# Optimization experiments

Hardware: AMD Instinct MI355X
Metric: run time of the kernel (lower is better)

The kernel has to match this reference:

```python
import jax, jax.numpy as jnp
import numpy as np

K_MASK = -2.3819763e+38
B, T, D = 1, 2048, 3584
N, KH, H = 28, 4, 128  # query heads, kv heads, head_dim
ROPE_THETA = 1000000.0


def _rope_tables(t, h, theta):
    pos = jnp.arange(t, dtype=jnp.float32)[:, None]
    freq = theta ** (-jnp.arange(0, h, 2, dtype=jnp.float32) / h)[None, :]
    ang = pos * freq  # (T, H/2)
    return jnp.sin(ang)[None], jnp.cos(ang)[None]  # (1, T, H/2)


def apply_rotary_embedding(x, sin, cos):
    # x: (B,T,heads,H); sin/cos: (B,T,H/2)
    x1, x2 = x[..., : x.shape[-1] // 2], x[..., x.shape[-1] // 2 :]
    s, c = sin[:, :, None, :], cos[:, :, None, :]
    return jnp.concatenate([x1 * c - x2 * s, x2 * c + x1 * s], axis=-1)


def setup_inputs() -> dict:
    key = jax.random.key(0)
    ks = jax.random.split(key, 8)
    x = jax.random.normal(ks[0], (B, T, D), jnp.float32)
    attn_mask = jnp.tril(jnp.ones((T, T), jnp.bool_))[None]  # causal (B,T,S)
    sin, cos = _rope_tables(T, H, ROPE_THETA)
    std = 0.02
    wq = jax.random.normal(ks[1], (D, N, H), jnp.float32) * std
    wk = jax.random.normal(ks[2], (D, KH, H), jnp.float32) * std
    wv = jax.random.normal(ks[3], (D, KH, H), jnp.float32) * std
    wo = jax.random.normal(ks[4], (N, H, D), jnp.float32) * std
    q_bias = jax.random.normal(ks[5], (N * H,), jnp.float32) * std
    k_bias = jax.random.normal(ks[6], (KH * H,), jnp.float32) * std
    v_bias = jax.random.normal(ks[7], (KH * H,), jnp.float32) * std
    return {"x": x, "attn_mask": attn_mask, "sin": sin, "cos": cos,
            "wq": wq, "wk": wk, "wv": wv, "wo": wo,
            "q_bias": q_bias, "k_bias": k_bias, "v_bias": v_bias}


def reference(x, attn_mask, sin, cos, wq, wk, wv, wo, q_bias, k_bias, v_bias):
    b, t, _ = x.shape
    q = jnp.einsum('BTD,DNH->BTNH', x, wq) + q_bias.reshape(1, 1, N, H)
    k = jnp.einsum('BSD,DKH->BSKH', x, wk) + k_bias.reshape(1, 1, KH, H)
    v = jnp.einsum('BSD,DKH->BSKH', x, wv) + v_bias.reshape(1, 1, KH, H)
    q = apply_rotary_embedding(q, sin, cos)
    k = apply_rotary_embedding(k, sin, cos)
    g = N // KH  # GQA group size
    scale = H ** -0.5
    qg = q.reshape(b, t, KH, g, H)
    attn = jnp.einsum('BTHGD,BSHD->BHGTS', qg, k) * scale  # no KV repetition
    attn = attn.reshape(b, N, t, t)
    attn = jnp.where(attn_mask[:, None, :, :], attn, K_MASK)
    attn = jax.nn.softmax(attn.astype(jnp.float32), axis=-1).astype(k.dtype)
    attn = attn.reshape(b, KH, g, t, t)
    qkv = jnp.einsum('BHGTS,BSHD->BTHGD', attn, v).reshape(b, t, N, H)
    return jnp.einsum('BTNH,NHD->BTD', qkv, wo)
```

## Files before the change

kernel.cpp:

```cpp
#include <hip/hip_runtime.h>
#include <hip/hip_bf16.h>
#include <math.h>

#define Tn 2048
#define Dn 3584
#define NH 28
#define KHn 4
#define Hn 128
#define Gn 7
#define SCALE 0.08838834764831845f
#define LDC 4608
#define KOFF 3584
#define VOFF 4096
#define FBQ 128
#define FBS 64
#define MAXT 8
#define EXP_SHIFT 12.0f

typedef unsigned short u16;
typedef __attribute__((ext_vector_type(8))) short short8;
typedef __attribute__((ext_vector_type(4))) float floatx4;

__device__ __constant__ unsigned char QT_TAB[40] = {
    15,15,15,15, 14,14,14, 13,13,13, 12,12,12, 11,11,11,
    10,10, 9,9, 8,8, 7,7, 6, 5, 4, 3,
    14,10,6,2, 13,9,5,1, 12,8,4,0};
__device__ __constant__ unsigned char S_TAB[40] = {
     0, 1, 2, 3,  0, 1, 2,  0, 1, 2,  0, 1, 2,  0, 1, 2,
     0, 1, 0,1, 0,1, 0,1, 0, 0, 0, 0,
     3, 2,1,0,  3,2,1,0,  3,2,1,0};

__device__ __forceinline__ float bf_lo(unsigned int u) {
    union { unsigned int i; float f; } x; x.i = u << 16; return x.f;
}
__device__ __forceinline__ u16 f2bf(float f) {
    __hip_bfloat16 h = __float2bfloat16(f);
    return *reinterpret_cast<u16*>(&h);
}

__global__ void cast_f32_bf16(const float* __restrict__ in, u16* __restrict__ out, int n4)
{
    const int idx = blockIdx.x * blockDim.x + threadIdx.x;
    if (idx >= n4) return;
    const float4 f = ((const float4*)in)[idx];
    ((ushort4*)out)[idx] = make_ushort4(f2bf(f.x), f2bf(f.y), f2bf(f.z), f2bf(f.w));
}

__global__ void zero_f32(float* __restrict__ p, int n)
{
    const int i = blockIdx.x * blockDim.x + threadIdx.x;
    if (i < n) p[i] = 0.f;
}

__global__ __launch_bounds__(256) void transpose_cast(
    const float* __restrict__ in, u16* __restrict__ out, int R, int C, int ldo)
{
    __shared__ float ts[32][33];
    const int tid = threadIdx.x;
    const int c0 = blockIdx.x * 32, r0 = blockIdx.y * 32;
    const int tx = tid & 31, ty = tid >> 5;
    #pragma unroll
    for (int i = 0; i < 4; ++i)
        ts[ty + i * 8][tx] = in[(size_t)(r0 + ty + i * 8) * C + c0 + tx];
    __syncthreads();
    #pragma unroll
    for (int i = 0; i < 4; ++i)
        out[(size_t)(c0 + ty + i * 8) * ldo + r0 + tx] = f2bf(ts[tx][ty + i * 8]);
}

__global__ __launch_bounds__(256) void transpose_v(
    const u16* __restrict__ qkv, u16* __restrict__ vt)
{
    __shared__ u16 ts[32][33];
    const int tid = threadIdx.x;
    const int s0 = blockIdx.x * 32, d0 = blockIdx.y * 32;
    const int tx = tid & 31, ty = tid >> 5;
    #pragma unroll
    for (int i = 0; i < 4; ++i)
        ts[ty + i * 8][tx] = qkv[(size_t)(s0 + ty + i * 8) * LDC + VOFF + d0 + tx];
    __syncthreads();
    #pragma unroll
    for (int i = 0; i < 4; ++i)
        vt[(size_t)(d0 + ty + i * 8) * Tn + s0 + tx] = ts[tx][ty + i * 8];
}

__global__ void concat_bias(const float* __restrict__ qb, const float* __restrict__ kb,
                            const float* __restrict__ vb, float* __restrict__ out)
{
    const int j = blockIdx.x * blockDim.x + threadIdx.x;
    if (j >= 4608) return;
    out[j] = j < 3584 ? qb[j] : (j < 4096 ? kb[j - 3584] : vb[j - 4096]);
}

#define GM 128
#define GN 128
#define GK 32

__device__ __forceinline__ void async16(const void* g, void* l) {
    __builtin_amdgcn_global_load_lds(
        (const __attribute__((address_space(1))) unsigned int*)g,
        (__attribute__((address_space(3))) unsigned int*)l, 16, 0, 0);
}

template <typename OUT_T>
__global__ __launch_bounds__(256) void gemm_bf16_mfma(
    const u16* __restrict__ A, const u16* __restrict__ Bt,
    const float* __restrict__ bias, OUT_T* __restrict__ C,
    int M, int N, int K, int ldc)
{
    __shared__ __align__(16) u16 As[GM * GK];
    __shared__ __align__(16) u16 Bs[GN * GK];

    const int tid  = threadIdx.x;
    const int lane = tid & 63;
    const int wave = tid >> 6;
    const int wr = wave >> 1, wc = wave & 1;
    const int m16 = lane & 15, quad = lane >> 4;

    const int nwg = gridDim.x * gridDim.y;
    const int bid = blockIdx.y * gridDim.x + blockIdx.x;
    const int cpx = nwg >> 3;
    const int swz = (bid & 7) * cpx + (bid >> 3);
    const int bm = (swz / gridDim.x) * GM;
    const int bn = (swz % gridDim.x) * GN;

    floatx4 acc[4][4];
    #pragma unroll
    for (int i = 0; i < 4; ++i)
        #pragma unroll
        for (int j = 0; j < 4; ++j) acc[i][j] = (floatx4)0.f;

    const int rl   = lane >> 2;
    const int kcol = (lane & 3) * 8;

    for (int k0 = 0; k0 < K; k0 += GK) {
        __syncthreads();
        #pragma unroll
        for (int i = 0; i < 2; ++i) {
            const int c = wave + i * 4;
            const int row = c * 16 + rl;
            async16(A  + (size_t)(bm + row) * K + k0 + kcol, &As[c * 512]);
            async16(Bt + (size_t)(bn + row) * K + k0 + kcol, &Bs[c * 512]);
        }
        __builtin_amdgcn_s_waitcnt(0);
        __syncthreads();

        short8 af[4], bfr[4];
        #pragma unroll
        for (int i = 0; i < 4; ++i)
            af[i] = *(const short8*)&As[(wr * 64 + i * 16 + m16) * GK + quad * 8];
        #pragma unroll
        for (int j = 0; j < 4; ++j)
            bfr[j] = *(const short8*)&Bs[(wc * 64 + j * 16 + m16) * GK + quad * 8];
        #pragma unroll
        for (int i = 0; i < 4; ++i)
            #pragma unroll
            for (int j = 0; j < 4; ++j)
                acc[i][j] = __builtin_amdgcn_mfma_f32_16x16x32_bf16(
                    af[i], bfr[j], acc[i][j], 0, 0, 0);
    }

    #pragma unroll
    for (int j = 0; j < 4; ++j) {
        const int col = bn + wc * 64 + j * 16 + m16;
        const float bv = bias ? bias[col] : 0.f;
        #pragma unroll
        for (int i = 0; i < 4; ++i) {
            const int rbase = bm + wr * 64 + i * 16 + quad * 4;
            #pragma unroll
            for (int r = 0; r < 4; ++r) {
                const float v = acc[i][j][r] + bv;
                if constexpr (sizeof(OUT_T) == 2)
                    C[(size_t)(rbase + r) * ldc + col] = (OUT_T)f2bf(v);
                else
                    C[(size_t)(rbase + r) * ldc + col] = v;
            }
        }
    }
}

__global__ void rope_bf16(u16* __restrict__ base,
                          const float* __restrict__ sin_t,
                          const float* __restrict__ cos_t,
                          int heads)
{
    const int idx = blockIdx.x * blockDim.x + threadIdx.x;
    const int n_elem = Tn * heads * 64;
    if (idx >= n_elem) return;
    const int i = idx & 63;
    const int h = (idx >> 6) % heads;
    const int t = idx / (64 * heads);
    const float s = sin_t[t * 64 + i];
    const float c = cos_t[t * 64 + i];
    u16* p = base + (size_t)t * LDC + h * Hn;
    const float x1 = bf_lo((unsigned int)p[i]);
    const float x2 = bf_lo((unsigned int)p[i + 64]);
    p[i]      = f2bf(x1 * c - x2 * s);
    p[i + 64] = f2bf(x2 * c + x1 * s);
}

__global__ __launch_bounds__(256, 2) void flash_attn_mfma(
    const u16* __restrict__ qkv, const u16* __restrict__ vt,
    u16* __restrict__ pb01, u16* __restrict__ pb23,
    float* __restrict__ lb)
{
    const int qt = (int)QT_TAB[blockIdx.x];
    const int s  = (int)S_TAB[blockIdx.x];
    const int n  = blockIdx.y;
    const int kh = n / Gn;
    const int tid  = threadIdx.x;
    const int lane = tid & 63;
    const int w    = tid >> 6;
    const int m16  = lane & 15;
    const int quad = lane >> 4;

    __shared__ __align__(16) u16 smem[64 * 136 + 128 * 72 + 128 * 72];
    u16* Ks = smem;
    u16* Vs = smem + 64 * 136;
    u16* Ps = Vs + 128 * 72;

    short8 qf[2][4];
    #pragma unroll
    for (int p = 0; p < 2; ++p) {
        const int qrow = qt * FBQ + w * 32 + p * 16 + m16;
        const u16* qp = qkv + (size_t)qrow * LDC + n * Hn;
        #pragma unroll
        for (int kc = 0; kc < 4; ++kc)
            qf[p][kc] = *(const short8*)(qp + kc * 32 + quad * 8);
    }

    floatx4 oacc[2][8];
    #pragma unroll
    for (int p = 0; p < 2; ++p)
        #pragma unroll
        for (int jn = 0; jn < 8; ++jn) oacc[p][jn] = (floatx4)0.f;
    float lrow[2][4];
    #pragma unroll
    for (int p = 0; p < 2; ++p)
        #pragma unroll
        for (int r = 0; r < 4; ++r) lrow[p][r] = 0.f;

    const int krow = tid >> 2, kseg = tid & 3;
    const int vrow = tid >> 1, vseg = tid & 1;
    const int nst = 2 * qt + 2;
    const int st0 = s * MAXT;
    const int st1 = (st0 + MAXT < nst) ? st0 + MAXT : nst;

    uint4 kv[4], vv[4];
    {
        const u16* kp = qkv + (size_t)(st0 * FBS + krow) * LDC + KOFF + kh * Hn + kseg * 32;
        #pragma unroll
        for (int i = 0; i < 4; ++i) kv[i] = *(const uint4*)(kp + i * 8);
        const u16* vp = vt + (size_t)(kh * Hn + vrow) * Tn + st0 * FBS + vseg * 32;
        #pragma unroll
        for (int i = 0; i < 4; ++i) vv[i] = *(const uint4*)(vp + i * 8);
    }

    for (int st = st0; st < st1; ++st) {
        __syncthreads();
        #pragma unroll
        for (int i = 0; i < 4; ++i)
            *(uint4*)&Ks[krow * 136 + kseg * 32 + i * 8] = kv[i];
        #pragma unroll
        for (int i = 0; i < 4; ++i)
            *(uint4*)&Vs[vrow * 72 + vseg * 32 + i * 8] = vv[i];
        __syncthreads();

        {
            const int pst = (st + 1 < st1) ? st + 1 : st1 - 1;
            const u16* kp = qkv + (size_t)(pst * FBS + krow) * LDC + KOFF + kh * Hn + kseg * 32;
            #pragma unroll
            for (int i = 0; i < 4; ++i) kv[i] = *(const uint4*)(kp + i * 8);
            const u16* vp = vt + (size_t)(kh * Hn + vrow) * Tn + pst * FBS + vseg * 32;
            #pragma unroll
            for (int i = 0; i < 4; ++i) vv[i] = *(const uint4*)(vp + i * 8);
        }

        const bool active = (st * FBS) <= (qt * FBQ + w * 32 + 31);
        if (active) {
            floatx4 sacc[2][4];
            #pragma unroll
            for (int p = 0; p < 2; ++p)
                #pragma unroll
                for (int j = 0; j < 4; ++j) sacc[p][j] = (floatx4)0.f;
            #pragma unroll
            for (int j = 0; j < 4; ++j) {
                #pragma unroll
                for (int kc = 0; kc < 4; ++kc) {
                    const short8 bfv = *(const short8*)&Ks[(j * 16 + m16) * 136 + kc * 32 + quad * 8];
                    sacc[0][j] = __builtin_amdgcn_mfma_f32_16x16x32_bf16(qf[0][kc], bfv, sacc[0][j], 0, 0, 0);
                    sacc[1][j] = __builtin_amdgcn_mfma_f32_16x16x32_bf16(qf[1][kc], bfv, sacc[1][j], 0, 0, 0);
                }
            }

            const bool diag = (st >= 2 * qt);
            #pragma unroll
            for (int p = 0; p < 2; ++p) {
                #pragma unroll
                for (int r = 0; r < 4; ++r) {
                    const int prow = w * 32 + p * 16 + quad * 4 + r;
                    const int row  = qt * FBQ + prow;
                    float ls = 0.f;
                    #pragma unroll
                    for (int j = 0; j < 4; ++j) {
                        float sv = sacc[p][j][r] * SCALE - EXP_SHIFT;
                        if (diag && (st * FBS + j * 16 + m16 > row)) sv = -1.0e30f;
                        const float e = __expf(sv);
                        ls += e;
                        Ps[prow * 72 + j * 16 + m16] = f2bf(e);
                    }
                    lrow[p][r] += ls;
                }
            }

            #pragma unroll
            for (int kc2 = 0; kc2 < 2; ++kc2) {
                const short8 af0 = *(const short8*)&Ps[(w * 32 + m16) * 72 + kc2 * 32 + quad * 8];
                const short8 af1 = *(const short8*)&Ps[(w * 32 + 16 + m16) * 72 + kc2 * 32 + quad * 8];
                #pragma unroll
                for (int jn = 0; jn < 8; ++jn) {
                    const short8 bfv = *(const short8*)&Vs[(jn * 16 + m16) * 72 + kc2 * 32 + quad * 8];
                    oacc[0][jn] = __builtin_amdgcn_mfma_f32_16x16x32_bf16(af0, bfv, oacc[0][jn], 0, 0, 0);
                    oacc[1][jn] = __builtin_amdgcn_mfma_f32_16x16x32_bf16(af1, bfv, oacc[1][jn], 0, 0, 0);
                }
            }
        }
    }

    float lsum[2][4], invl[2][4];
    #pragma unroll
    for (int p = 0; p < 2; ++p)
        #pragma unroll
        for (int r = 0; r < 4; ++r) {
            float l = lrow[p][r];
            l += __shfl_xor(l, 1); l += __shfl_xor(l, 2);
            l += __shfl_xor(l, 4); l += __shfl_xor(l, 8);
            lsum[p][r] = l;
            invl[p][r] = (l > 0.f) ? 1.0f / l : 0.f;
        }

    if (m16 == 0) {
        #pragma unroll
        for (int p = 0; p < 2; ++p)
            #pragma unroll
            for (int r = 0; r < 4; ++r) {
                const int row = qt * FBQ + w * 32 + p * 16 + quad * 4 + r;
                lb[((size_t)s * NH + n) * Tn + row] = lsum[p][r];
            }
    }

    u16* po = (s < 2) ? pb01 + (size_t)s * Tn * Dn
                      : pb23 + (size_t)(s - 2) * Tn * Dn;
    #pragma unroll
    for (int p = 0; p < 2; ++p)
        #pragma unroll
        for (int r = 0; r < 4; ++r) {
            const int grow = qt * FBQ + w * 32 + p * 16 + quad * 4 + r;
            u16* pr = po + (size_t)grow * Dn + n * Hn + m16;
            #pragma unroll
            for (int jn = 0; jn < 8; ++jn)
                pr[jn * 16] = f2bf(oacc[p][jn][r] * invl[p][r]);
        }
}

__global__ __launch_bounds__(256) void combine_splits(
    const u16* __restrict__ pb01, const u16* __restrict__ pb23,
    const float* __restrict__ lb, u16* __restrict__ ob)
{
    const int idx = blockIdx.x * blockDim.x + threadIdx.x;
    const int n4  = Tn * Dn / 4;
    if (idx >= n4) return;
    const int c4  = idx % (Dn / 4);
    const int row = idx / (Dn / 4);
    const int n   = (c4 * 4) >> 7;

    float den = 0.f, ax = 0.f, ay = 0.f, az = 0.f, aw = 0.f;
    #pragma unroll
    for (int s = 0; s < 4; ++s) {
        const float l = lb[((size_t)s * NH + n) * Tn + row];
        if (l > 0.f) {
            const u16* p = (s < 2) ? pb01 + (size_t)s * Tn * Dn
                                   : pb23 + (size_t)(s - 2) * Tn * Dn;
            const ushort4 v = ((const ushort4*)p)[idx];
            den += l;
            ax += l * bf_lo((unsigned int)v.x);
            ay += l * bf_lo((unsigned int)v.y);
            az += l * bf_lo((unsigned int)v.z);
            aw += l * bf_lo((unsigned int)v.w);
        }
    }
    const float inv = 1.0f / den;
    ushort4 o;
    o.x = f2bf(ax * inv);
    o.y = f2bf(ay * inv);
    o.z = f2bf(az * inv);
    o.w = f2bf(aw * inv);
    ((ushort4*)ob)[idx] = o;
}

extern "C" void kernel_launch(void* const* d_in, const int* in_sizes, int n_in,
                              void* d_out, int out_size, void* d_ws, size_t ws_size,
                              hipStream_t stream)
{
    const float* x      = (const float*)d_in[0];
    const float* sin_t  = (const float*)d_in[2];
    const float* cos_t  = (const float*)d_in[3];
    const float* wq     = (const float*)d_in[4];
    const float* wk     = (const float*)d_in[5];
    const float* wv     = (const float*)d_in[6];
    const float* wo     = (const float*)d_in[7];
    const float* q_bias = (const float*)d_in[8];
    const float* k_bias = (const float*)d_in[9];
    const float* v_bias = (const float*)d_in[10];
    float* out = (float*)d_out;

    char* ws = (char*)d_ws;
    u16*  cqkv = (u16*)ws;
    u16*  abuf = (u16*)(ws + 18874368);
    u16*  wt   = (u16*)(ws + 18874368 + 14680064);
    float* bqkv = (float*)(ws + 66584576);
    u16*  vtg  = wt;
    u16*  pb01 = (u16*)d_out;
    u16*  pb23 = (u16*)(ws + 35651584);
    float* lbf = (float*)(ws + 65011712);
    u16*  xb   = (u16*)d_out;

    cast_f32_bf16<<<(Tn * Dn / 4 + 255) / 256, 256, 0, stream>>>(x, xb, Tn * Dn / 4);
    transpose_cast<<<dim3(Dn / 32, Dn / 32), 256, 0, stream>>>(wq, wt, Dn, Dn, Dn);
    transpose_cast<<<dim3(512 / 32, Dn / 32), 256, 0, stream>>>(wk, wt + (size_t)KOFF * Dn, Dn, 512, Dn);
    transpose_cast<<<dim3(512 / 32, Dn / 32), 256, 0, stream>>>(wv, wt + (size_t)VOFF * Dn, Dn, 512, Dn);
    concat_bias<<<18, 256, 0, stream>>>(q_bias, k_bias, v_bias, bqkv);

    gemm_bf16_mfma<u16><<<dim3(LDC / GN, Tn / GM), 256, 0, stream>>>(
        xb, wt, bqkv, cqkv, Tn, LDC, Dn, LDC);

    zero_f32<<<(4 * NH * Tn + 255) / 256, 256, 0, stream>>>(lbf, 4 * NH * Tn);

    rope_bf16<<<(Tn * 32 * 64 + 255) / 256, 256, 0, stream>>>(cqkv, sin_t, cos_t, 32);

    transpose_v<<<dim3(Tn / 32, 512 / 32), 256, 0, stream>>>(cqkv, vtg);

    flash_attn_mfma<<<dim3(40, NH), 256, 0, stream>>>(
        cqkv, vtg, pb01, pb23, lbf);

    combine_splits<<<(Tn * Dn / 4 + 255) / 256, 256, 0, stream>>>(pb01, pb23, lbf, abuf);

    transpose_cast<<<dim3(Dn / 32, Dn / 32), 256, 0, stream>>>(wo, wt, Dn, Dn, Dn);
    gemm_bf16_mfma<float><<<dim3(Dn / GN, Tn / GM), 256, 0, stream>>>(
        abuf, wt, nullptr, out, Tn, Dn, Dn, Dn);
}
```

Measured before the change: 562.2 us.

## Load K/V MFMA fragments directly from global and stage output stores through LDS

The flash-attention kernel no longer copies K and V tiles into shared memory. Each wave now loads its MFMA B-operand fragments straight from global memory, which removes the two per-tile __syncthreads and the register prefetch, and shrinks shared memory to the P buffer. The epilogue now writes normalized outputs into that P buffer per wave, then emits coalesced 16-byte row stores instead of scattered 2-byte stores. The cost is that all four waves re-fetch the same K/V data through the cache with strided, less coalesced accesses, and there is no explicit prefetch to hide that latency.

Result: slower. 579.0 us (+3.0%).

```diff
diff --git a/kernel.cpp b/kernel.cpp
--- a/kernel.cpp
+++ b/kernel.cpp
@@ -214,10 +214,7 @@
     const int m16  = lane & 15;
     const int quad = lane >> 4;
 
-    __shared__ __align__(16) u16 smem[64 * 136 + 128 * 72 + 128 * 72];
-    u16* Ks = smem;
-    u16* Vs = smem + 64 * 136;
-    u16* Ps = Vs + 128 * 72;
+    __shared__ __align__(16) u16 Ps[128 * 72];
 
     short8 qf[2][4];
     #pragma unroll
@@ -240,89 +237,63 @@
         #pragma unroll
         for (int r = 0; r < 4; ++r) lrow[p][r] = 0.f;
 
-    const int krow = tid >> 2, kseg = tid & 3;
-    const int vrow = tid >> 1, vseg = tid & 1;
     const int nst = 2 * qt + 2;
     const int st0 = s * MAXT;
     const int st1 = (st0 + MAXT < nst) ? st0 + MAXT : nst;
 
-    uint4 kv[4], vv[4];
-    {
-        const u16* kp = qkv + (size_t)(st0 * FBS + krow) * LDC + KOFF + kh * Hn + kseg * 32;
-        #pragma unroll
-        for (int i = 0; i < 4; ++i) kv[i] = *(const uint4*)(kp + i * 8);
-        const u16* vp = vt + (size_t)(kh * Hn + vrow) * Tn + st0 * FBS + vseg * 32;
-        #pragma unroll
-        for (int i = 0; i < 4; ++i) vv[i] = *(const uint4*)(vp + i * 8);
-    }
+    const u16* kfrag = qkv + (size_t)m16 * LDC + KOFF + kh * Hn + quad * 8;
+    const u16* vfrag = vt + (size_t)(kh * Hn + m16) * Tn + quad * 8;
 
     for (int st = st0; st < st1; ++st) {
-        __syncthreads();
-        #pragma unroll
-        for (int i = 0; i < 4; ++i)
-            *(uint4*)&Ks[krow * 136 + kseg * 32 + i * 8] = kv[i];
-        #pragma unroll
-        for (int i = 0; i < 4; ++i)
-            *(uint4*)&Vs[vrow * 72 + vseg * 32 + i * 8] = vv[i];
-        __syncthreads();
-
-        {
-            const int pst = (st + 1 < st1) ? st + 1 : st1 - 1;
-            const u16* kp = qkv + (size_t)(pst * FBS + krow) * LDC + KOFF + kh * Hn + kseg * 32;
-            #pragma unroll
-            for (int i = 0; i < 4; ++i) kv[i] = *(const uint4*)(kp + i * 8);
-            const u16* vp = vt + (size_t)(kh * Hn + vrow) * Tn + pst * FBS + vseg * 32;
-            #pragma unroll
-            for (int i = 0; i < 4; ++i) vv[i] = *(const uint4*)(vp + i * 8);
-        }
-
-        const bool active = (st * FBS) <= (qt * FBQ + w * 32 + 31);
-        if (active) {
-            floatx4 sacc[2][4];
-            #pragma unroll
-            for (int p = 0; p < 2; ++p)
+        if ((st * FBS) > (qt * FBQ + w * 32 + 31)) continue;
+
+        const u16* kb = kfrag + (size_t)(st * FBS) * LDC;
+        const u16* vb = vfrag + st * FBS;
+
+        floatx4 sacc[2][4];
+        #pragma unroll
+        for (int j = 0; j < 4; ++j) sacc[0][j] = (floatx4)0.f;
+        #pragma unroll
+        for (int j = 0; j < 4; ++j) sacc[1][j] = (floatx4)0.f;
+        #pragma unroll
+        for (int j = 0; j < 4; ++j) {
+            #pragma unroll
+            for (int kc = 0; kc < 4; ++kc) {
+                const short8 bfv = *(const short8*)(kb + (size_t)(j * 16) * LDC + kc * 32);
+                sacc[0][j] = __builtin_amdgcn_mfma_f32_16x16x32_bf16(qf[0][kc], bfv, sacc[0][j], 0, 0, 0);
+                sacc[1][j] = __builtin_amdgcn_mfma_f32_16x16x32_bf16(qf[1][kc], bfv, sacc[1][j], 0, 0, 0);
+            }
+        }
+
+        const bool diag = (st >= 2 * qt);
+        #pragma unroll
+        for (int p = 0; p < 2; ++p) {
+            #pragma unroll
+            for (int r = 0; r < 4; ++r) {
+                const int prow = w * 32 + p * 16 + quad * 4 + r;
+                const int row  = qt * FBQ + prow;
+                float ls = 0.f;
                 #pragma unroll
-                for (int j = 0; j < 4; ++j) sacc[p][j] = (floatx4)0.f;
-            #pragma unroll
-            for (int j = 0; j < 4; ++j) {
-                #pragma unroll
-                for (int kc = 0; kc < 4; ++kc) {
-                    const short8 bfv = *(const short8*)&Ks[(j * 16 + m16) * 136 + kc * 32 + quad * 8];
-                    sacc[0][j] = __builtin_amdgcn_mfma_f32_16x16x32_bf16(qf[0][kc], bfv, sacc[0][j], 0, 0, 0);
-                    sacc[1][j] = __builtin_amdgcn_mfma_f32_16x16x32_bf16(qf[1][kc], bfv, sacc[1][j], 0, 0, 0);
+                for (int j = 0; j < 4; ++j) {
+                    float sv = sacc[p][j][r] * SCALE - EXP_SHIFT;
+                    if (diag && (st * FBS + j * 16 + m16 > row)) sv = -1.0e30f;
+                    const float e = __expf(sv);
+                    ls += e;
+                    Ps[prow * 72 + j * 16 + m16] = f2bf(e);
                 }
-            }
-
-            const bool diag = (st >= 2 * qt);
-            #pragma unroll
-            for (int p = 0; p < 2; ++p) {
-                #pragma unroll
-                for (int r = 0; r < 4; ++r) {
-                    const int prow = w * 32 + p * 16 + quad * 4 + r;
-                    const int row  = qt * FBQ + prow;
-                    float ls = 0.f;
-                    #pragma unroll
-                    for (int j = 0; j < 4; ++j) {
-                        float sv = sacc[p][j][r] * SCALE - EXP_SHIFT;
-                        if (diag && (st * FBS + j * 16 + m16 > row)) sv = -1.0e30f;
-                        const float e = __expf(sv);
-                        ls += e;
-                        Ps[prow * 72 + j * 16 + m16] = f2bf(e);
-                    }
-                    lrow[p][r] += ls;
-                }
-            }
-
-            #pragma unroll
-            for (int kc2 = 0; kc2 < 2; ++kc2) {
-                const short8 af0 = *(const short8*)&Ps[(w * 32 + m16) * 72 + kc2 * 32 + quad * 8];
-                const short8 af1 = *(const short8*)&Ps[(w * 32 + 16 + m16) * 72 + kc2 * 32 + quad * 8];
-                #pragma unroll
-                for (int jn = 0; jn < 8; ++jn) {
-                    const short8 bfv = *(const short8*)&Vs[(jn * 16 + m16) * 72 + kc2 * 32 + quad * 8];
-                    oacc[0][jn] = __builtin_amdgcn_mfma_f32_16x16x32_bf16(af0, bfv, oacc[0][jn], 0, 0, 0);
-                    oacc[1][jn] = __builtin_amdgcn_mfma_f32_16x16x32_bf16(af1, bfv, oacc[1][jn], 0, 0, 0);
-                }
+                lrow[p][r] += ls;
+            }
+        }
+
+        #pragma unroll
+        for (int kc2 = 0; kc2 < 2; ++kc2) {
+            const short8 af0 = *(const short8*)&Ps[(w * 32 + m16) * 72 + kc2 * 32 + quad * 8];
+            const short8 af1 = *(const short8*)&Ps[(w * 32 + 16 + m16) * 72 + kc2 * 32 + quad * 8];
+            #pragma unroll
+            for (int jn = 0; jn < 8; ++jn) {
+                const short8 bfv = *(const short8*)(vb + (size_t)(jn * 16) * Tn + kc2 * 32);
+                oacc[0][jn] = __builtin_amdgcn_mfma_f32_16x16x32_bf16(af0, bfv, oacc[0][jn], 0, 0, 0);
+                oacc[1][jn] = __builtin_amdgcn_mfma_f32_16x16x32_bf16(af1, bfv, oacc[1][jn], 0, 0, 0);
             }
         }
     }
@@ -351,16 +322,27 @@
 
     u16* po = (s < 2) ? pb01 + (size_t)s * Tn * Dn
                       : pb23 + (size_t)(s - 2) * Tn * Dn;
-    #pragma unroll
-    for (int p = 0; p < 2; ++p)
-        #pragma unroll
-        for (int r = 0; r < 4; ++r) {
-            const int grow = qt * FBQ + w * 32 + p * 16 + quad * 4 + r;
-            u16* pr = po + (size_t)grow * Dn + n * Hn + m16;
-            #pragma unroll
-            for (int jn = 0; jn < 8; ++jn)
-                pr[jn * 16] = f2bf(oacc[p][jn][r] * invl[p][r]);
-        }
+    const int orow_l = w * 32 + (lane >> 1);
+    const int seg    = lane & 1;
+    #pragma unroll
+    for (int h = 0; h < 2; ++h) {
+        #pragma unroll
+        for (int p = 0; p < 2; ++p)
+            #pragma unroll
+            for (int r = 0; r < 4; ++r) {
+                const int mrw = w * 32 + p * 16 + quad * 4 + r;
+                #pragma unroll
+                for (int j4 = 0; j4 < 4; ++j4)
+                    Ps[mrw * 72 + j4 * 16 + m16] =
+                        f2bf(oacc[p][h * 4 + j4][r] * invl[p][r]);
+            }
+        u16* orow = po + (size_t)(qt * FBQ + orow_l) * Dn + n * Hn + h * 64 + seg * 32;
+        #pragma unroll
+        for (int i = 0; i < 4; ++i) {
+            const uint4 d = *(const uint4*)&Ps[orow_l * 72 + seg * 32 + i * 8];
+            *(uint4*)(orow + i * 8) = d;
+        }
+    }
 }
 
 __global__ __launch_bounds__(256) void combine_splits(
```
